# Kernel tuning notes

Measured on AMD Instinct MI355X. Metric: run time of the kernel, lower is better.

## Reference

```python
import jax, jax.numpy as jnp
import numpy as np

EMBED = 1024
HEADS = 16
HEAD_DIM = EMBED // HEADS


def setup_inputs() -> dict:
    key = jax.random.key(0)
    ks = jax.random.split(key, 5)
    s = 1.0 / np.sqrt(EMBED)
    return {
        "x": jax.random.normal(ks[0], (4, 2048, EMBED), dtype=jnp.float32),
        "W_qkv": jax.random.uniform(ks[1], (EMBED, 3 * EMBED), jnp.float32, -s, s),
        "b_qkv": jax.random.uniform(ks[2], (3 * EMBED,), jnp.float32, -s, s),
        "W_out": jax.random.uniform(ks[3], (EMBED, EMBED), jnp.float32, -s, s),
        "b_out": jax.random.uniform(ks[4], (EMBED,), jnp.float32, -s, s),
    }


def reference(x, W_qkv, b_qkv, W_out, b_out):
    B, S, E = x.shape
    qkv = x @ W_qkv + b_qkv  # [B,S,3E]
    q, k, v = jnp.split(qkv, 3, axis=-1)
    # [B,S,E] -> [B,H,S,D]
    def split_heads(t):
        return t.reshape(B, S, HEADS, HEAD_DIM).transpose(0, 2, 1, 3)
    q, k, v = split_heads(q), split_heads(k), split_heads(v)
    scale = 1.0 / jnp.sqrt(jnp.asarray(HEAD_DIM, dtype=x.dtype))
    scores = jnp.einsum("bhqd,bhkd->bhqk", q, k) * scale
    attn = jax.nn.softmax(scores, axis=-1)
    out = jnp.einsum("bhqk,bhkd->bhqd", attn, v)
    out = out.transpose(0, 2, 1, 3).reshape(B, S, E)
    return out @ W_out + b_out
```

## Files before the change

kernel.cpp:

```cpp
#include <hip/hip_runtime.h>
#include <hip/hip_bf16.h>

typedef __bf16 bf16;
typedef __bf16 bf16x8 __attribute__((ext_vector_type(8)));
typedef float f32x4 __attribute__((ext_vector_type(4)));

#define EMB 1024
#define SEQ 2048
#define NH 16
#define HD 64
#define MTOK 8192

__global__ __launch_bounds__(256) void cast_f32_bf16(const float* __restrict__ in,
                                                     bf16* __restrict__ out, int n8) {
    int i = blockIdx.x * blockDim.x + threadIdx.x;
    if (i < n8) {
        const float4* p = (const float4*)in + 2 * (size_t)i;
        float4 a = p[0], b = p[1];
        bf16x8 v;
        v[0] = (bf16)a.x; v[1] = (bf16)a.y; v[2] = (bf16)a.z; v[3] = (bf16)a.w;
        v[4] = (bf16)b.x; v[5] = (bf16)b.y; v[6] = (bf16)b.z; v[7] = (bf16)b.w;
        *(bf16x8*)(out + 8 * (size_t)i) = v;
    }
}

__global__ __launch_bounds__(256) void transpose_cast(const float* __restrict__ W,
                                                      bf16* __restrict__ Wt, int K, int N) {
    __shared__ float tile[32][33];
    int n0 = blockIdx.x * 32, k0 = blockIdx.y * 32;
    int tx = threadIdx.x & 31, ty = threadIdx.x >> 5;
    #pragma unroll
    for (int i = 0; i < 32; i += 8)
        tile[ty + i][tx] = W[(size_t)(k0 + ty + i) * N + n0 + tx];
    __syncthreads();
    #pragma unroll
    for (int i = 0; i < 32; i += 8)
        Wt[(size_t)(n0 + ty + i) * K + k0 + tx] = (bf16)tile[tx][ty + i];
}

#define BM 128
#define BN 128
#define BK 64
#define LDK 72

#define QSCALE 0.1803368801111f

__global__ __launch_bounds__(256) void gemm_qkv(const bf16* __restrict__ A,
                                                const bf16* __restrict__ Bt,
                                                const float* __restrict__ bias,
                                                bf16* __restrict__ qws, bf16* __restrict__ kws,
                                                bf16* __restrict__ vt) {
    __shared__ bf16 sA[BM][LDK];
    __shared__ bf16 sB[BN][LDK];
    const int K = 1024;
    int m0 = blockIdx.x * BM, n0 = blockIdx.y * BN;
    int t = threadIdx.x, lane = t & 63, w = t >> 6;
    int wr = w >> 1, wc = w & 1;
    int l15 = lane & 15, quad = lane >> 4;

    f32x4 acc[4][4];
    #pragma unroll
    for (int i = 0; i < 4; i++)
        #pragma unroll
        for (int j = 0; j < 4; j++) acc[i][j] = (f32x4){0.f, 0.f, 0.f, 0.f};

    int srow = t >> 3, sc8 = (t & 7) * 8;
    for (int kt = 0; kt < K; kt += BK) {
        #pragma unroll
        for (int p = 0; p < 4; p++) {
            int r = srow + p * 32;
            *(uint4*)&sA[r][sc8] = *(const uint4*)(A + (size_t)(m0 + r) * K + kt + sc8);
            *(uint4*)&sB[r][sc8] = *(const uint4*)(Bt + (size_t)(n0 + r) * K + kt + sc8);
        }
        __syncthreads();
        #pragma unroll
        for (int ks = 0; ks < BK; ks += 32) {
            int kk = ks + quad * 8;
            bf16x8 af[4], bfr[4];
            #pragma unroll
            for (int mt = 0; mt < 4; mt++) af[mt] = *(const bf16x8*)&sA[wr * 64 + mt * 16 + l15][kk];
            #pragma unroll
            for (int nt = 0; nt < 4; nt++) bfr[nt] = *(const bf16x8*)&sB[wc * 64 + nt * 16 + l15][kk];
            #pragma unroll
            for (int mt = 0; mt < 4; mt++)
                #pragma unroll
                for (int nt = 0; nt < 4; nt++)
                    acc[mt][nt] = __builtin_amdgcn_mfma_f32_16x16x32_bf16(af[mt], bfr[nt], acc[mt][nt], 0, 0, 0);
        }
        __syncthreads();
    }
    #pragma unroll
    for (int mt = 0; mt < 4; mt++)
        #pragma unroll
        for (int nt = 0; nt < 4; nt++) {
            int col = n0 + wc * 64 + nt * 16 + l15;
            float bv = bias[col];
            int mat = col >> 10;
            int e = col & 1023;
            int h = e >> 6, d = e & 63;
            int row0 = m0 + wr * 64 + mt * 16 + quad * 4;
            int bb = row0 >> 11, s0 = row0 & 2047;
            int bh = bb * NH + h;
            float vv[4];
            #pragma unroll
            for (int r = 0; r < 4; r++) vv[r] = acc[mt][nt][r] + bv;
            if (mat == 0) {
                #pragma unroll
                for (int r = 0; r < 4; r++)
                    qws[((size_t)bh * SEQ + s0 + r) * HD + d] = (bf16)(vv[r] * QSCALE);
            } else if (mat == 1) {
                #pragma unroll
                for (int r = 0; r < 4; r++)
                    kws[((size_t)bh * SEQ + s0 + r) * HD + d] = (bf16)vv[r];
            } else {
                ushort4 pk;
                pk.x = __builtin_bit_cast(unsigned short, (bf16)vv[0]);
                pk.y = __builtin_bit_cast(unsigned short, (bf16)vv[1]);
                pk.z = __builtin_bit_cast(unsigned short, (bf16)vv[2]);
                pk.w = __builtin_bit_cast(unsigned short, (bf16)vv[3]);
                *(ushort4*)((unsigned short*)vt + ((size_t)bh * HD + d) * SEQ + s0) = pk;
            }
        }
}

#define PQP 68
__global__ __launch_bounds__(256, 4) void attn(const bf16* __restrict__ qws, const bf16* __restrict__ kws,
                                               const bf16* __restrict__ vt, bf16* __restrict__ ao) {
    __shared__ bf16 sK[64][72];
    __shared__ bf16 sVt[64][72];
    __shared__ bf16 sPq[128][PQP];

    int q0 = blockIdx.x * 128, bh = blockIdx.y;
    int t = threadIdx.x, lane = t & 63, w = t >> 6;
    int l15 = lane & 15, quad = lane >> 4;

    const bf16* qb = qws + (size_t)bh * SEQ * HD;
    const bf16* kb = kws + (size_t)bh * SEQ * HD;
    const bf16* vtb = vt + (size_t)bh * HD * SEQ;

    bf16x8 qf[2][2];
    #pragma unroll
    for (int nq = 0; nq < 2; nq++)
        #pragma unroll
        for (int ks = 0; ks < 2; ks++)
            qf[nq][ks] = *(const bf16x8*)(qb + (size_t)(q0 + w * 32 + nq * 16 + l15) * HD + ks * 32 + quad * 8);

    f32x4 o[4][2];
    float lsum[2] = {0.f, 0.f};
    #pragma unroll
    for (int mt = 0; mt < 4; mt++)
        #pragma unroll
        for (int nq = 0; nq < 2; nq++) o[mt][nq] = (f32x4){0.f, 0.f, 0.f, 0.f};

    int krow = t >> 3, kc8 = (t & 7) * 8;
    int vdr = t >> 2, vc16 = (t & 3) * 16;

    for (int kv0 = 0; kv0 < SEQ; kv0 += 64) {
        #pragma unroll
        for (int p = 0; p < 2; p++) {
            int r = krow + p * 32;
            *(uint4*)&sK[r][kc8] = *(const uint4*)(kb + (size_t)(kv0 + r) * HD + kc8);
        }
        {
            const bf16* src = vtb + (size_t)vdr * SEQ + kv0 + vc16;
            *(uint4*)&sVt[vdr][vc16] = *(const uint4*)src;
            *(uint4*)&sVt[vdr][vc16 + 8] = *(const uint4*)(src + 8);
        }
        __syncthreads();

        f32x4 sacc[4][2];
        #pragma unroll
        for (int nt = 0; nt < 4; nt++)
            #pragma unroll
            for (int nq = 0; nq < 2; nq++) sacc[nt][nq] = (f32x4){0.f, 0.f, 0.f, 0.f};
        #pragma unroll
        for (int ks = 0; ks < 2; ks++) {
            #pragma unroll
            for (int nt = 0; nt < 4; nt++) {
                bf16x8 kf = *(const bf16x8*)&sK[nt * 16 + l15][ks * 32 + quad * 8];
                #pragma unroll
                for (int nq = 0; nq < 2; nq++)
                    sacc[nt][nq] = __builtin_amdgcn_mfma_f32_16x16x32_bf16(kf, qf[nq][ks], sacc[nt][nq], 0, 0, 0);
            }
        }

        #pragma unroll
        for (int nt = 0; nt < 4; nt++)
            #pragma unroll
            for (int nq = 0; nq < 2; nq++) {
                float p0 = __builtin_amdgcn_exp2f(sacc[nt][nq][0]);
                float p1 = __builtin_amdgcn_exp2f(sacc[nt][nq][1]);
                float p2 = __builtin_amdgcn_exp2f(sacc[nt][nq][2]);
                float p3 = __builtin_amdgcn_exp2f(sacc[nt][nq][3]);
                lsum[nq] += (p0 + p1) + (p2 + p3);
                unsigned int u0 = (unsigned int)__builtin_bit_cast(unsigned short, (bf16)p0) |
                                  ((unsigned int)__builtin_bit_cast(unsigned short, (bf16)p1) << 16);
                unsigned int u1 = (unsigned int)__builtin_bit_cast(unsigned short, (bf16)p2) |
                                  ((unsigned int)__builtin_bit_cast(unsigned short, (bf16)p3) << 16);
                *(uint2*)&sPq[w * 32 + nq * 16 + l15][nt * 16 + quad * 4] = make_uint2(u0, u1);
            }
        __threadfence_block();

        #pragma unroll
        for (int ks2 = 0; ks2 < 2; ks2++) {
            bf16x8 pb[2];
            #pragma unroll
            for (int nq = 0; nq < 2; nq++) {
                const bf16* pr = &sPq[w * 32 + nq * 16 + l15][ks2 * 32 + quad * 8];
                uint2 lo = *(const uint2*)pr;
                uint2 hi = *(const uint2*)(pr + 4);
                uint4 uv; uv.x = lo.x; uv.y = lo.y; uv.z = hi.x; uv.w = hi.y;
                pb[nq] = __builtin_bit_cast(bf16x8, uv);
            }
            #pragma unroll
            for (int mt = 0; mt < 4; mt++) {
                bf16x8 vf = *(const bf16x8*)&sVt[mt * 16 + l15][ks2 * 32 + quad * 8];
                #pragma unroll
                for (int nq = 0; nq < 2; nq++)
                    o[mt][nq] = __builtin_amdgcn_mfma_f32_16x16x32_bf16(vf, pb[nq], o[mt][nq], 0, 0, 0);
            }
        }
        __syncthreads();
    }

    float inv[2];
    #pragma unroll
    for (int nq = 0; nq < 2; nq++) {
        float s = lsum[nq];
        s += __shfl_xor(s, 16);
        s += __shfl_xor(s, 32);
        inv[nq] = __builtin_amdgcn_rcpf(s);
    }

    int h = bh & 15, bb = bh >> 4;
    #pragma unroll
    for (int mt = 0; mt < 4; mt++)
        #pragma unroll
        for (int nq = 0; nq < 2; nq++) {
            int srow = q0 + w * 32 + nq * 16 + l15;
            int col = h * HD + mt * 16 + quad * 4;
            ushort4 pk;
            pk.x = __builtin_bit_cast(unsigned short, (bf16)(o[mt][nq][0] * inv[nq]));
            pk.y = __builtin_bit_cast(unsigned short, (bf16)(o[mt][nq][1] * inv[nq]));
            pk.z = __builtin_bit_cast(unsigned short, (bf16)(o[mt][nq][2] * inv[nq]));
            pk.w = __builtin_bit_cast(unsigned short, (bf16)(o[mt][nq][3] * inv[nq]));
            *(ushort4*)((unsigned short*)ao + ((size_t)(bb * SEQ + srow)) * EMB + col) = pk;
        }
}

__global__ __launch_bounds__(256) void gemm_out(const bf16* __restrict__ A,
                                                const bf16* __restrict__ Bt,
                                                const float* __restrict__ bias,
                                                float* __restrict__ out) {
    __shared__ bf16 sA[BM][LDK];
    __shared__ bf16 sB[BN][LDK];
    const int K = 1024;
    int m0 = blockIdx.x * BM, n0 = blockIdx.y * BN;
    int t = threadIdx.x, lane = t & 63, w = t >> 6;
    int wr = w >> 1, wc = w & 1;
    int l15 = lane & 15, quad = lane >> 4;

    f32x4 acc[4][4];
    #pragma unroll
    for (int i = 0; i < 4; i++)
        #pragma unroll
        for (int j = 0; j < 4; j++) acc[i][j] = (f32x4){0.f, 0.f, 0.f, 0.f};

    int srow = t >> 3, sc8 = (t & 7) * 8;
    for (int kt = 0; kt < K; kt += BK) {
        #pragma unroll
        for (int p = 0; p < 4; p++) {
            int r = srow + p * 32;
            *(uint4*)&sA[r][sc8] = *(const uint4*)(A + (size_t)(m0 + r) * K + kt + sc8);
            *(uint4*)&sB[r][sc8] = *(const uint4*)(Bt + (size_t)(n0 + r) * K + kt + sc8);
        }
        __syncthreads();
        #pragma unroll
        for (int ks = 0; ks < BK; ks += 32) {
            int kk = ks + quad * 8;
            bf16x8 af[4], bfr[4];
            #pragma unroll
            for (int mt = 0; mt < 4; mt++) af[mt] = *(const bf16x8*)&sA[wr * 64 + mt * 16 + l15][kk];
            #pragma unroll
            for (int nt = 0; nt < 4; nt++) bfr[nt] = *(const bf16x8*)&sB[wc * 64 + nt * 16 + l15][kk];
            #pragma unroll
            for (int mt = 0; mt < 4; mt++)
                #pragma unroll
                for (int nt = 0; nt < 4; nt++)
                    acc[mt][nt] = __builtin_amdgcn_mfma_f32_16x16x32_bf16(af[mt], bfr[nt], acc[mt][nt], 0, 0, 0);
        }
        __syncthreads();
    }
    #pragma unroll
    for (int mt = 0; mt < 4; mt++)
        #pragma unroll
        for (int nt = 0; nt < 4; nt++) {
            int col = n0 + wc * 64 + nt * 16 + l15;
            float bv = bias[col];
            #pragma unroll
            for (int r = 0; r < 4; r++) {
                int row = m0 + wr * 64 + mt * 16 + quad * 4 + r;
                out[(size_t)row * EMB + col] = acc[mt][nt][r] + bv;
            }
        }
}

extern "C" void kernel_launch(void* const* d_in, const int* in_sizes, int n_in,
                              void* d_out, int out_size, void* d_ws, size_t ws_size,
                              hipStream_t stream) {
    const float* x     = (const float*)d_in[0];
    const float* W_qkv = (const float*)d_in[1];
    const float* b_qkv = (const float*)d_in[2];
    const float* W_out = (const float*)d_in[3];
    const float* b_out = (const float*)d_in[4];
    float* out = (float*)d_out;

    char* ws = (char*)d_ws;
    bf16* xb    = (bf16*)(ws);
    bf16* wqkvT = (bf16*)(ws + (size_t)(16 << 20));
    bf16* woutT = (bf16*)(ws + (size_t)(22 << 20));
    bf16* qws   = (bf16*)(ws + (size_t)(24 << 20));
    bf16* kws   = (bf16*)(ws + (size_t)(40 << 20));
    bf16* vt    = (bf16*)(ws + (size_t)(56 << 20));
    bf16* aow   = (bf16*)(ws + (size_t)(72 << 20));

    cast_f32_bf16<<<4096, 256, 0, stream>>>(x, xb, MTOK * EMB / 8);
    transpose_cast<<<dim3(3 * EMB / 32, EMB / 32), 256, 0, stream>>>(W_qkv, wqkvT, EMB, 3 * EMB);
    transpose_cast<<<dim3(EMB / 32, EMB / 32), 256, 0, stream>>>(W_out, woutT, EMB, EMB);
    gemm_qkv<<<dim3(MTOK / BM, 3 * EMB / BN), 256, 0, stream>>>(xb, wqkvT, b_qkv, qws, kws, vt);
    attn<<<dim3(SEQ / 128, 64), 256, 0, stream>>>(qws, kws, vt, aow);
    gemm_out<<<dim3(MTOK / BM, EMB / BN), 256, 0, stream>>>(aow, woutT, b_out, out);
}
```

Before: 285.1 us.

## Switch attention to 32x32x16 MFMA with register-resident P and 256-query tiles

Rewrites the attention kernel to use 32x32x16 bf16 MFMA tiles instead of 16x16x32. The probability matrix now stays in registers, converted to the B-operand layout with cross-half-wave shuffles, so the shared-memory staging buffer and its fence go away. Each block now handles 256 queries (64 per wave), which halves how often K/V tiles are reloaded per query. The cost is more accumulator registers, dropped occupancy hints and only half as many blocks, which may hurt latency hiding.

```diff
diff --git a/kernel.cpp b/kernel.cpp
--- a/kernel.cpp
+++ b/kernel.cpp
@@ -4,6 +4,7 @@
 typedef __bf16 bf16;
 typedef __bf16 bf16x8 __attribute__((ext_vector_type(8)));
 typedef float f32x4 __attribute__((ext_vector_type(4)));
+typedef float f32x16 __attribute__((ext_vector_type(16)));
 
 #define EMB 1024
 #define SEQ 2048
@@ -123,34 +124,40 @@
         }
 }
 
-#define PQP 68
-__global__ __launch_bounds__(256, 4) void attn(const bf16* __restrict__ qws, const bf16* __restrict__ kws,
-                                               const bf16* __restrict__ vt, bf16* __restrict__ ao) {
+__device__ __forceinline__ unsigned pk2(float a, float b) {
+    unsigned lo = (unsigned)__builtin_bit_cast(unsigned short, (bf16)a);
+    unsigned hi = (unsigned)__builtin_bit_cast(unsigned short, (bf16)b);
+    return lo | (hi << 16);
+}
+
+__global__ __launch_bounds__(256) void attn(const bf16* __restrict__ qws, const bf16* __restrict__ kws,
+                                            const bf16* __restrict__ vt, bf16* __restrict__ ao) {
     __shared__ bf16 sK[64][72];
     __shared__ bf16 sVt[64][72];
-    __shared__ bf16 sPq[128][PQP];
-
-    int q0 = blockIdx.x * 128, bh = blockIdx.y;
+
+    int q0 = blockIdx.x * 256, bh = blockIdx.y;
     int t = threadIdx.x, lane = t & 63, w = t >> 6;
-    int l15 = lane & 15, quad = lane >> 4;
+    int l31 = lane & 31, hi = lane >> 5;
 
     const bf16* qb = qws + (size_t)bh * SEQ * HD;
     const bf16* kb = kws + (size_t)bh * SEQ * HD;
     const bf16* vtb = vt + (size_t)bh * HD * SEQ;
 
-    bf16x8 qf[2][2];
+    bf16x8 qf[2][4];
     #pragma unroll
     for (int nq = 0; nq < 2; nq++)
         #pragma unroll
-        for (int ks = 0; ks < 2; ks++)
-            qf[nq][ks] = *(const bf16x8*)(qb + (size_t)(q0 + w * 32 + nq * 16 + l15) * HD + ks * 32 + quad * 8);
-
-    f32x4 o[4][2];
+        for (int ks = 0; ks < 4; ks++)
+            qf[nq][ks] = *(const bf16x8*)(qb + (size_t)(q0 + w * 64 + nq * 32 + l31) * HD + ks * 16 + hi * 8);
+
+    f32x16 o[2][2];
     float lsum[2] = {0.f, 0.f};
     #pragma unroll
-    for (int mt = 0; mt < 4; mt++)
-        #pragma unroll
-        for (int nq = 0; nq < 2; nq++) o[mt][nq] = (f32x4){0.f, 0.f, 0.f, 0.f};
+    for (int mt = 0; mt < 2; mt++)
+        #pragma unroll
+        for (int nq = 0; nq < 2; nq++)
+            #pragma unroll
+            for (int r = 0; r < 16; r++) o[mt][nq][r] = 0.f;
 
     int krow = t >> 3, kc8 = (t & 7) * 8;
     int vdr = t >> 2, vc16 = (t & 3) * 16;
@@ -168,83 +175,84 @@
         }
         __syncthreads();
 
-        f32x4 sacc[4][2];
-        #pragma unroll
-        for (int nt = 0; nt < 4; nt++)
-            #pragma unroll
-            for (int nq = 0; nq < 2; nq++) sacc[nt][nq] = (f32x4){0.f, 0.f, 0.f, 0.f};
-        #pragma unroll
-        for (int ks = 0; ks < 2; ks++) {
-            #pragma unroll
-            for (int nt = 0; nt < 4; nt++) {
-                bf16x8 kf = *(const bf16x8*)&sK[nt * 16 + l15][ks * 32 + quad * 8];
+        f32x16 sacc[2][2];
+        #pragma unroll
+        for (int nt = 0; nt < 2; nt++)
+            #pragma unroll
+            for (int nq = 0; nq < 2; nq++)
+                #pragma unroll
+                for (int r = 0; r < 16; r++) sacc[nt][nq][r] = 0.f;
+        #pragma unroll
+        for (int ks = 0; ks < 4; ks++)
+            #pragma unroll
+            for (int nt = 0; nt < 2; nt++) {
+                bf16x8 kf = *(const bf16x8*)&sK[nt * 32 + l31][ks * 16 + hi * 8];
                 #pragma unroll
                 for (int nq = 0; nq < 2; nq++)
-                    sacc[nt][nq] = __builtin_amdgcn_mfma_f32_16x16x32_bf16(kf, qf[nq][ks], sacc[nt][nq], 0, 0, 0);
-            }
-        }
-
-        #pragma unroll
-        for (int nt = 0; nt < 4; nt++)
+                    sacc[nt][nq] = __builtin_amdgcn_mfma_f32_32x32x16_bf16(kf, qf[nq][ks], sacc[nt][nq], 0, 0, 0);
+            }
+
+        bf16x8 pb[2][4];
+        #pragma unroll
+        for (int nt = 0; nt < 2; nt++)
             #pragma unroll
             for (int nq = 0; nq < 2; nq++) {
-                float p0 = __builtin_amdgcn_exp2f(sacc[nt][nq][0]);
-                float p1 = __builtin_amdgcn_exp2f(sacc[nt][nq][1]);
-                float p2 = __builtin_amdgcn_exp2f(sacc[nt][nq][2]);
-                float p3 = __builtin_amdgcn_exp2f(sacc[nt][nq][3]);
-                lsum[nq] += (p0 + p1) + (p2 + p3);
-                unsigned int u0 = (unsigned int)__builtin_bit_cast(unsigned short, (bf16)p0) |
-                                  ((unsigned int)__builtin_bit_cast(unsigned short, (bf16)p1) << 16);
-                unsigned int u1 = (unsigned int)__builtin_bit_cast(unsigned short, (bf16)p2) |
-                                  ((unsigned int)__builtin_bit_cast(unsigned short, (bf16)p3) << 16);
-                *(uint2*)&sPq[w * 32 + nq * 16 + l15][nt * 16 + quad * 4] = make_uint2(u0, u1);
-            }
-        __threadfence_block();
-
-        #pragma unroll
-        for (int ks2 = 0; ks2 < 2; ks2++) {
-            bf16x8 pb[2];
-            #pragma unroll
-            for (int nq = 0; nq < 2; nq++) {
-                const bf16* pr = &sPq[w * 32 + nq * 16 + l15][ks2 * 32 + quad * 8];
-                uint2 lo = *(const uint2*)pr;
-                uint2 hi = *(const uint2*)(pr + 4);
-                uint4 uv; uv.x = lo.x; uv.y = lo.y; uv.z = hi.x; uv.w = hi.y;
-                pb[nq] = __builtin_bit_cast(bf16x8, uv);
-            }
-            #pragma unroll
-            for (int mt = 0; mt < 4; mt++) {
-                bf16x8 vf = *(const bf16x8*)&sVt[mt * 16 + l15][ks2 * 32 + quad * 8];
+                float e[16];
+                #pragma unroll
+                for (int r = 0; r < 16; r++) {
+                    e[r] = __builtin_amdgcn_exp2f(sacc[nt][nq][r]);
+                    lsum[nq] += e[r];
+                }
+                #pragma unroll
+                for (int blk = 0; blk < 2; blk++) {
+                    int b = blk * 8;
+                    unsigned x0 = pk2(e[b + 0], e[b + 1]), x1 = pk2(e[b + 2], e[b + 3]);
+                    unsigned y0 = pk2(e[b + 4], e[b + 5]), y1 = pk2(e[b + 6], e[b + 7]);
+                    unsigned r0 = __shfl_xor(hi ? x0 : y0, 32);
+                    unsigned r1 = __shfl_xor(hi ? x1 : y1, 32);
+                    uint4 f;
+                    f.x = hi ? r0 : x0;
+                    f.y = hi ? r1 : x1;
+                    f.z = hi ? y0 : r0;
+                    f.w = hi ? y1 : r1;
+                    pb[nq][nt * 2 + blk] = __builtin_bit_cast(bf16x8, f);
+                }
+            }
+
+        #pragma unroll
+        for (int s = 0; s < 4; s++)
+            #pragma unroll
+            for (int mt = 0; mt < 2; mt++) {
+                bf16x8 vf = *(const bf16x8*)&sVt[mt * 32 + l31][s * 16 + hi * 8];
                 #pragma unroll
                 for (int nq = 0; nq < 2; nq++)
-                    o[mt][nq] = __builtin_amdgcn_mfma_f32_16x16x32_bf16(vf, pb[nq], o[mt][nq], 0, 0, 0);
-            }
-        }
+                    o[mt][nq] = __builtin_amdgcn_mfma_f32_32x32x16_bf16(vf, pb[nq][s], o[mt][nq], 0, 0, 0);
+            }
         __syncthreads();
     }
 
     float inv[2];
     #pragma unroll
     for (int nq = 0; nq < 2; nq++) {
-        float s = lsum[nq];
-        s += __shfl_xor(s, 16);
-        s += __shfl_xor(s, 32);
+        float s = lsum[nq] + __shfl_xor(lsum[nq], 32);
         inv[nq] = __builtin_amdgcn_rcpf(s);
     }
 
     int h = bh & 15, bb = bh >> 4;
     #pragma unroll
-    for (int mt = 0; mt < 4; mt++)
+    for (int mt = 0; mt < 2; mt++)
         #pragma unroll
         for (int nq = 0; nq < 2; nq++) {
-            int srow = q0 + w * 32 + nq * 16 + l15;
-            int col = h * HD + mt * 16 + quad * 4;
-            ushort4 pk;
-            pk.x = __builtin_bit_cast(unsigned short, (bf16)(o[mt][nq][0] * inv[nq]));
-            pk.y = __builtin_bit_cast(unsigned short, (bf16)(o[mt][nq][1] * inv[nq]));
-            pk.z = __builtin_bit_cast(unsigned short, (bf16)(o[mt][nq][2] * inv[nq]));
-            pk.w = __builtin_bit_cast(unsigned short, (bf16)(o[mt][nq][3] * inv[nq]));
-            *(ushort4*)((unsigned short*)ao + ((size_t)(bb * SEQ + srow)) * EMB + col) = pk;
+            int q = q0 + w * 64 + nq * 32 + l31;
+            #pragma unroll
+            for (int g = 0; g < 4; g++) {
+                ushort4 pk;
+                pk.x = __builtin_bit_cast(unsigned short, (bf16)(o[mt][nq][4 * g + 0] * inv[nq]));
+                pk.y = __builtin_bit_cast(unsigned short, (bf16)(o[mt][nq][4 * g + 1] * inv[nq]));
+                pk.z = __builtin_bit_cast(unsigned short, (bf16)(o[mt][nq][4 * g + 2] * inv[nq]));
+                pk.w = __builtin_bit_cast(unsigned short, (bf16)(o[mt][nq][4 * g + 3] * inv[nq]));
+                *(ushort4*)((unsigned short*)ao + ((size_t)(bb * SEQ + q)) * EMB + h * HD + mt * 32 + 8 * g + 4 * hi) = pk;
+            }
         }
 }
 
@@ -328,6 +336,6 @@
     transpose_cast<<<dim3(3 * EMB / 32, EMB / 32), 256, 0, stream>>>(W_qkv, wqkvT, EMB, 3 * EMB);
     transpose_cast<<<dim3(EMB / 32, EMB / 32), 256, 0, stream>>>(W_out, woutT, EMB, EMB);
     gemm_qkv<<<dim3(MTOK / BM, 3 * EMB / BN), 256, 0, stream>>>(xb, wqkvT, b_qkv, qws, kws, vt);
-    attn<<<dim3(SEQ / 128, 64), 256, 0, stream>>>(qws, kws, vt, aow);
+    attn<<<dim3(SEQ / 256, 64), 256, 0, stream>>>(qws, kws, vt, aow);
     gemm_out<<<dim3(MTOK / BM, EMB / BN), 256, 0, stream>>>(aow, woutT, b_out, out);
 }
```

Result: slower. 307.9 us (+8.0%).
